# Kernel optimization log

Hardware: AMD Instinct MI355X
Metric: run time of the kernel (lower is better)

## Reference

```python
import jax, jax.numpy as jnp
import numpy as np

B, T, EMB, HEAD = 8, 2048, 1024, 1024

def setup_inputs() -> dict:
    key = jax.random.key(0)
    k1, k2, k3, k4 = jax.random.split(key, 4)
    s = 1.0 / np.sqrt(EMB)
    return {
        "x": jax.random.normal(k1, (B, T, EMB), dtype=jnp.float32),
        "Wq": jax.random.normal(k2, (HEAD, EMB), dtype=jnp.float32) * s,
        "Wk": jax.random.normal(k3, (HEAD, EMB), dtype=jnp.float32) * s,
        "Wv": jax.random.normal(k4, (HEAD, EMB), dtype=jnp.float32) * s,
    }

def reference(x, Wq, Wk, Wv):
    # Bias-free projections; torch Linear weight is [out, in] -> contract on last dim.
    q = jnp.einsum('btc,hc->bth', x, Wq)  # [B,T,HEAD]
    k = jnp.einsum('btc,hc->bth', x, Wk)
    v = jnp.einsum('btc,hc->bth', x, Wv)
    C = x.shape[-1]
    scale = jnp.asarray(C, x.dtype) ** -0.5  # NOTE: scales by emb dim C, as in source
    wei = jnp.einsum('bth,bsh->bts', q, k) * scale  # [B,T,T]
    Tn = x.shape[1]
    causal = jnp.tril(jnp.ones((Tn, Tn), dtype=bool))
    wei = jnp.where(causal, wei, -jnp.inf)
    wei = jax.nn.softmax(wei, axis=-1)
    # dropout omitted (eval mode / deterministic reference)
    out = jnp.einsum('bts,bsh->bth', wei, v)  # [B,T,HEAD]
    return out
```

## Files before the change

kernel.cpp:

```cpp
#include <hip/hip_runtime.h>

typedef unsigned short u16;
typedef short short8 __attribute__((ext_vector_type(8)));
typedef float f32x4 __attribute__((ext_vector_type(4)));

__device__ __forceinline__ u16 f2bf(float f) {
    union { float f; unsigned u; } c; c.f = f;
    unsigned r = c.u + 0x7fffu + ((c.u >> 16) & 1u);
    return (u16)(r >> 16);
}
__device__ __forceinline__ float bf2f(u16 h) {
    union { unsigned u; float f; } c; c.u = ((unsigned)h) << 16; return c.f;
}

__device__ __forceinline__ void gll16(const u16* g, u16* l) {
    __builtin_amdgcn_global_load_lds(
        (const __attribute__((address_space(1))) void*)g,
        (__attribute__((address_space(3))) void*)l, 16, 0, 0);
}

__device__ __forceinline__ void stage_half(const u16* __restrict__ g, int ld,
                                           u16* lds, int w, int lane) {
    int rowl = w * 16 + (lane >> 3);
    int s = lane & 7;
    gll16(g + (size_t)rowl * ld + ((s ^ (rowl & 7)) << 3), lds + (w * 2) * 512);
    rowl += 8;
    gll16(g + (size_t)rowl * ld + ((s ^ (rowl & 7)) << 3), lds + (w * 2 + 1) * 512);
}

__device__ __forceinline__ short8 ldsfrag(const u16* h, int row, int slot) {
    return *reinterpret_cast<const short8*>(h + row * 64 + ((slot ^ (row & 7)) << 3));
}

__device__ __forceinline__ void gemm256(
    const u16* __restrict__ A, int lda,
    const u16* __restrict__ B, int ldb,
    int m0, int n0, int nk,
    u16* Ab, u16* Bb, f32x4 acc[8][4])
{
    const int tid  = threadIdx.x;
    const int lane = tid & 63;
    const int w    = tid >> 6;
    const int wm   = w >> 2;
    const int wn   = w & 3;
    const int kg   = lane >> 4, l15 = lane & 15;

    const u16* Am = A + (size_t)m0 * lda;
    const u16* Bn = B + (size_t)n0 * ldb;

    stage_half(Am,                       lda, Ab + 0 * 8192, w, lane);
    stage_half(Am + (size_t)128 * lda,   lda, Ab + 1 * 8192, w, lane);
    stage_half(Bn,                       ldb, Bb + 0 * 8192, w, lane);
    stage_half(Bn + (size_t)128 * ldb,   ldb, Bb + 1 * 8192, w, lane);
    if (nk > 1) {
        stage_half(Bn + 64,                     ldb, Bb + 2 * 8192, w, lane);
        stage_half(Bn + (size_t)128 * ldb + 64, ldb, Bb + 3 * 8192, w, lane);
        asm volatile("s_waitcnt vmcnt(4)" ::: "memory");
    } else {
        asm volatile("s_waitcnt vmcnt(0)" ::: "memory");
    }
    __builtin_amdgcn_s_barrier();

    for (int t = 0; t < nk; ++t) {
        const int p = t & 1;
        const u16* Ahalf = Ab + (p * 2 + wm) * 8192;
        const u16* Bhalf = Bb + (p * 2 + (wn >> 1)) * 8192;
        const int brow0 = (wn & 1) * 64;
        short8 bfr[4][2];

        #pragma unroll
        for (int mp = 0; mp < 4; ++mp) {
            short8 a[2][2];
            #pragma unroll
            for (int mi = 0; mi < 2; ++mi)
                #pragma unroll
                for (int ks = 0; ks < 2; ++ks)
                    a[mi][ks] = ldsfrag(Ahalf, (mp * 2 + mi) * 16 + l15, ks * 4 + kg);
            if (mp == 0) {
                #pragma unroll
                for (int nt = 0; nt < 4; ++nt)
                    #pragma unroll
                    for (int ks = 0; ks < 2; ++ks)
                        bfr[nt][ks] = ldsfrag(Bhalf, brow0 + nt * 16 + l15, ks * 4 + kg);
            }
            if (mp == 0 && t + 1 < nk)
                stage_half(Am + (t + 1) * 64, lda, Ab + ((p ^ 1) * 2 + 0) * 8192, w, lane);
            if (mp == 1 && t + 1 < nk)
                stage_half(Am + (size_t)128 * lda + (t + 1) * 64, lda, Ab + ((p ^ 1) * 2 + 1) * 8192, w, lane);
            if (mp == 2 && t + 2 < nk)
                stage_half(Bn + (t + 2) * 64, ldb, Bb + (p * 2 + 0) * 8192, w, lane);
            if (mp == 3 && t + 2 < nk)
                stage_half(Bn + (size_t)128 * ldb + (t + 2) * 64, ldb, Bb + (p * 2 + 1) * 8192, w, lane);

            __builtin_amdgcn_s_barrier();
            __builtin_amdgcn_s_setprio(1);
            #pragma unroll
            for (int ks = 0; ks < 2; ++ks)
                #pragma unroll
                for (int mi = 0; mi < 2; ++mi)
                    #pragma unroll
                    for (int nt = 0; nt < 4; ++nt)
                        acc[mp * 2 + mi][nt] = __builtin_amdgcn_mfma_f32_16x16x32_bf16(
                            a[mi][ks], bfr[nt][ks], acc[mp * 2 + mi][nt], 0, 0, 0);
            __builtin_amdgcn_s_setprio(0);
            if (mp == 3) {
                if (t + 2 < nk) asm volatile("s_waitcnt vmcnt(4)" ::: "memory");
                else            asm volatile("s_waitcnt vmcnt(0)" ::: "memory");
            }
            __builtin_amdgcn_s_barrier();
        }
    }
}

__global__ __launch_bounds__(256) void cvt_bf16(
    const float* __restrict__ x,
    const float* __restrict__ Wq,
    const float* __restrict__ Wk,
    const float* __restrict__ Wv,
    u16* __restrict__ dst)
{
    const size_t e = ((size_t)blockIdx.x * 256 + threadIdx.x) * 8;
    const float* src;
    if (e < (size_t)16777216) {
        src = x + e;
    } else {
        size_t j = e - 16777216;
        int z = (int)(j >> 20);
        const float* Wz = (z == 0) ? Wq : (z == 1) ? Wk : Wv;
        src = Wz + (j & 1048575);
    }
    float4 a = *reinterpret_cast<const float4*>(src);
    float4 b = *reinterpret_cast<const float4*>(src + 4);
    short8 v;
    v[0] = (short)f2bf(a.x); v[1] = (short)f2bf(a.y);
    v[2] = (short)f2bf(a.z); v[3] = (short)f2bf(a.w);
    v[4] = (short)f2bf(b.x); v[5] = (short)f2bf(b.y);
    v[6] = (short)f2bf(b.z); v[7] = (short)f2bf(b.w);
    *reinterpret_cast<short8*>(dst + e) = v;
}

__global__ __launch_bounds__(512, 2) void qkv256(
    const u16* __restrict__ xb,
    const u16* __restrict__ Wb,
    u16* __restrict__ Qo, u16* __restrict__ Ko, u16* __restrict__ VTo)
{
    __shared__ u16 Ab[4][8192];
    __shared__ u16 Bb[4][8192];
    const int tid = threadIdx.x;
    const int lane = tid & 63, w = tid >> 6;
    const int wm = w >> 2, wn = w & 3, kg = lane >> 4, l15 = lane & 15;
    const int m0 = blockIdx.x * 256, n0 = blockIdx.y * 256, z = blockIdx.z;

    const f32x4 z4 = {0.f, 0.f, 0.f, 0.f};
    f32x4 acc[8][4];
    #pragma unroll
    for (int i = 0; i < 8; ++i)
        #pragma unroll
        for (int j = 0; j < 4; ++j) acc[i][j] = z4;

    gemm256(xb, 1024, Wb + (size_t)z * 1048576, 1024, m0, n0, 16, &Ab[0][0], &Bb[0][0], acc);

    if (z < 2) {
        u16* O = (z == 0) ? Qo : Ko;
        #pragma unroll
        for (int mt = 0; mt < 8; ++mt) {
            const int row0 = m0 + wm * 128 + mt * 16 + kg * 4;
            #pragma unroll
            for (int nt = 0; nt < 4; ++nt) {
                const int col = n0 + wn * 64 + nt * 16 + l15;
                #pragma unroll
                for (int r = 0; r < 4; ++r)
                    O[(size_t)(row0 + r) * 1024 + col] = f2bf(acc[mt][nt][r]);
            }
        }
    } else {
        #pragma unroll
        for (int mt = 0; mt < 8; ++mt) {
            const int row0 = m0 + wm * 128 + mt * 16 + kg * 4;
            #pragma unroll
            for (int nt = 0; nt < 4; ++nt) {
                const int col = n0 + wn * 64 + nt * 16 + l15;
                #pragma unroll
                for (int r = 0; r < 4; ++r) {
                    const int rr = row0 + r;
                    VTo[((size_t)(rr >> 11) * 1024 + col) * 2048 + (rr & 2047)] = f2bf(acc[mt][nt][r]);
                }
            }
        }
    }
}

__global__ __launch_bounds__(512, 2) void sp256(
    const u16* __restrict__ Q, const u16* __restrict__ K, u16* __restrict__ P)
{
    const int qb = blockIdx.x, kb = blockIdx.y, b = blockIdx.z;
    if (kb > qb) return;
    __shared__ u16 Ab[4][8192];
    __shared__ u16 Bb[4][8192];
    const int tid = threadIdx.x;
    const int lane = tid & 63, w = tid >> 6;
    const int wm = w >> 2, wn = w & 3, kg = lane >> 4, l15 = lane & 15;

    const f32x4 z4 = {0.f, 0.f, 0.f, 0.f};
    f32x4 acc[8][4];
    #pragma unroll
    for (int i = 0; i < 8; ++i)
        #pragma unroll
        for (int j = 0; j < 4; ++j) acc[i][j] = z4;

    gemm256(Q, 1024, K, 1024, b * 2048 + qb * 256, b * 2048 + kb * 256, 16,
            &Ab[0][0], &Bb[0][0], acc);

    u16* Pb = P + (size_t)b * 2048 * 2048;
    #pragma unroll
    for (int mt = 0; mt < 8; ++mt) {
        const int trow0 = qb * 256 + wm * 128 + mt * 16 + kg * 4;
        #pragma unroll
        for (int nt = 0; nt < 4; ++nt) {
            const int scol = kb * 256 + wn * 64 + nt * 16 + l15;
            #pragma unroll
            for (int r = 0; r < 4; ++r) {
                const int trow = trow0 + r;
                const float p = (scol <= trow) ? __expf(acc[mt][nt][r] * 0.03125f) : 0.f;
                Pb[(size_t)trow * 2048 + scol] = f2bf(p);
            }
        }
    }
}

__global__ __launch_bounds__(512, 2) void pv256(
    const u16* __restrict__ P, const u16* __restrict__ VT, float* __restrict__ Of)
{
    const int b = blockIdx.x >> 3, qblk = blockIdx.x & 7;
    const int nb = blockIdx.y;
    const int nk = (qblk + 1) * 4;
    __shared__ u16 Ab[4][8192];
    __shared__ u16 Bb[4][8192];
    const int tid = threadIdx.x;
    const int lane = tid & 63, w = tid >> 6;
    const int wm = w >> 2, wn = w & 3, kg = lane >> 4, l15 = lane & 15;

    const f32x4 z4 = {0.f, 0.f, 0.f, 0.f};
    f32x4 acc[8][4];
    #pragma unroll
    for (int i = 0; i < 8; ++i)
        #pragma unroll
        for (int j = 0; j < 4; ++j) acc[i][j] = z4;

    gemm256(P + (size_t)b * 2048 * 2048, 2048,
            VT + (size_t)b * 1024 * 2048, 2048,
            qblk * 256, nb * 256, nk, &Ab[0][0], &Bb[0][0], acc);

    #pragma unroll
    for (int mt = 0; mt < 8; ++mt) {
        const int trow0 = qblk * 256 + wm * 128 + mt * 16 + kg * 4;
        #pragma unroll
        for (int nt = 0; nt < 4; ++nt) {
            const int col = nb * 256 + wn * 64 + nt * 16 + l15;
            #pragma unroll
            for (int r = 0; r < 4; ++r)
                Of[((size_t)b * 2048 + trow0 + r) * 1024 + col] = acc[mt][nt][r];
        }
    }
}

__global__ __launch_bounds__(256) void finalize(
    const u16* __restrict__ P, const float* __restrict__ Of, float* __restrict__ out)
{
    const int row = blockIdx.x;
    const int tid = threadIdx.x;
    const int b = row >> 11, t = row & 2047;
    const int len = ((t >> 8) + 1) * 256;
    const u16* prow = P + ((size_t)b * 2048 + t) * 2048;

    float s = 0.f;
    const int i = tid * 8;
    if (i < len) {
        short8 v = *reinterpret_cast<const short8*>(prow + i);
        #pragma unroll
        for (int j = 0; j < 8; ++j) s += bf2f((u16)v[j]);
    }
    #pragma unroll
    for (int d = 1; d < 64; d <<= 1) s += __shfl_xor(s, d, 64);

    __shared__ float red[4];
    if ((tid & 63) == 0) red[tid >> 6] = s;
    __syncthreads();
    const float rinv = 1.f / (red[0] + red[1] + red[2] + red[3]);

    const size_t o = (size_t)row * 1024 + tid * 4;
    f32x4 v = *reinterpret_cast<const f32x4*>(Of + o);
    v[0] *= rinv; v[1] *= rinv; v[2] *= rinv; v[3] *= rinv;
    *reinterpret_cast<f32x4*>(out + o) = v;
}

extern "C" void kernel_launch(void* const* d_in, const int* in_sizes, int n_in,
                              void* d_out, int out_size, void* d_ws, size_t ws_size,
                              hipStream_t stream) {
    const float* x  = (const float*)d_in[0];
    const float* Wq = (const float*)d_in[1];
    const float* Wk = (const float*)d_in[2];
    const float* Wv = (const float*)d_in[3];
    float* out = (float*)d_out;

    u16* Qb  = (u16*)d_ws;
    u16* Kb  = Qb + (size_t)16384 * 1024;
    u16* VTb = Kb + (size_t)16384 * 1024;
    float* Of = (float*)d_ws;

    u16* xb = (u16*)d_out;
    u16* Wb = xb + (size_t)16777216;
    u16* Pb = (u16*)d_out;

    cvt_bf16<<<dim3(9728), 256, 0, stream>>>(x, Wq, Wk, Wv, xb);
    qkv256<<<dim3(64, 4, 3), 512, 0, stream>>>(xb, Wb, Qb, Kb, VTb);
    sp256<<<dim3(8, 8, 8), 512, 0, stream>>>(Qb, Kb, Pb);
    pv256<<<dim3(64, 4), 512, 0, stream>>>(Pb, VTb, Of);
    finalize<<<dim3(16384), 256, 0, stream>>>(Pb, Of, out);
}
```

Measured before the change: 299.8 us.

## Rework GEMM pipeline to 4-stage BK=32 and store only causal P tiles

Replaces the double-buffered BK=64 GEMM core with a 4-buffer BK=32 pipeline that keeps two register fragment sets and prefetches three stages ahead. The score kernel now writes only the lower-triangular 256x256 P tiles into a packed workspace and emits per-tile row sums. A small rowsum kernel turns those into reciprocals, and the PV kernel applies them in its epilogue, which removes the separate finalize pass and the fp32 intermediate buffer. When the workspace is large enough, V is projected after the score stage so its buffer can reuse Q's space. This adds extra kernel launches and a workspace-size-dependent code path.

```diff
diff --git a/kernel.cpp b/kernel.cpp
--- a/kernel.cpp
+++ b/kernel.cpp
@@ -3,6 +3,12 @@
 typedef unsigned short u16;
 typedef short short8 __attribute__((ext_vector_type(8)));
 typedef float f32x4 __attribute__((ext_vector_type(4)));
+
+#define WS_K_OFF    33554432ULL
+#define WS_PTRI     67108864ULL
+#define WS_PART     104857600ULL
+#define WS_RINV     105381888ULL
+#define WS_NEED     105447424ULL
 
 __device__ __forceinline__ u16 f2bf(float f) {
     union { float f; unsigned u; } c; c.f = f;
@@ -12,103 +18,96 @@
 __device__ __forceinline__ float bf2f(u16 h) {
     union { unsigned u; float f; } c; c.u = ((unsigned)h) << 16; return c.f;
 }
-
 __device__ __forceinline__ void gll16(const u16* g, u16* l) {
     __builtin_amdgcn_global_load_lds(
         (const __attribute__((address_space(1))) void*)g,
         (__attribute__((address_space(3))) void*)l, 16, 0, 0);
 }
 
-__device__ __forceinline__ void stage_half(const u16* __restrict__ g, int ld,
-                                           u16* lds, int w, int lane) {
-    int rowl = w * 16 + (lane >> 3);
-    int s = lane & 7;
-    gll16(g + (size_t)rowl * ld + ((s ^ (rowl & 7)) << 3), lds + (w * 2) * 512);
-    rowl += 8;
-    gll16(g + (size_t)rowl * ld + ((s ^ (rowl & 7)) << 3), lds + (w * 2 + 1) * 512);
-}
-
-__device__ __forceinline__ short8 ldsfrag(const u16* h, int row, int slot) {
-    return *reinterpret_cast<const short8*>(h + row * 64 + ((slot ^ (row & 7)) << 3));
-}
-
-__device__ __forceinline__ void gemm256(
+template<int AMODE>
+__device__ __forceinline__ void gemm_pipe(
     const u16* __restrict__ A, int lda,
     const u16* __restrict__ B, int ldb,
-    int m0, int n0, int nk,
-    u16* Ab, u16* Bb, f32x4 acc[8][4])
+    int m0, int n0, int nk, u16* lds, f32x4 acc[8][4])
 {
     const int tid  = threadIdx.x;
     const int lane = tid & 63;
     const int w    = tid >> 6;
-    const int wm   = w >> 2;
-    const int wn   = w & 3;
+    const int wm   = w >> 2, wn = w & 3;
     const int kg   = lane >> 4, l15 = lane & 15;
-
-    const u16* Am = A + (size_t)m0 * lda;
-    const u16* Bn = B + (size_t)n0 * ldb;
-
-    stage_half(Am,                       lda, Ab + 0 * 8192, w, lane);
-    stage_half(Am + (size_t)128 * lda,   lda, Ab + 1 * 8192, w, lane);
-    stage_half(Bn,                       ldb, Bb + 0 * 8192, w, lane);
-    stage_half(Bn + (size_t)128 * ldb,   ldb, Bb + 1 * 8192, w, lane);
-    if (nk > 1) {
-        stage_half(Bn + 64,                     ldb, Bb + 2 * 8192, w, lane);
-        stage_half(Bn + (size_t)128 * ldb + 64, ldb, Bb + 3 * 8192, w, lane);
-        asm volatile("s_waitcnt vmcnt(4)" ::: "memory");
-    } else {
-        asm volatile("s_waitcnt vmcnt(0)" ::: "memory");
-    }
+    const int r0   = w * 32 + (lane >> 2);
+    const int s0   = (lane & 3) ^ ((r0 >> 1) & 3);
+
+    const int ldA = AMODE ? 256 : lda;
+    const u16* Ar0 = A + (size_t)(m0 + r0) * ldA + s0 * 8;
+    const u16* Ar1 = Ar0 + 16 * ldA;
+    const u16* Br0 = B + (size_t)(n0 + r0) * ldb + s0 * 8;
+    const u16* Br1 = Br0 + 16 * ldb;
+
+    auto aoff = [&](int t) -> int {
+        return AMODE ? ((t >> 3) * 65536 + (t & 7) * 32) : t * 32;
+    };
+    auto STAGE = [&](int t) {
+        const int ao = aoff(t), bo = t * 32, buf = (t & 3) * 16384;
+        u16* dA = lds + buf + w * 1024;
+        u16* dB = lds + buf + 8192 + w * 1024;
+        gll16(Ar0 + ao, dA);
+        gll16(Ar1 + ao, dA + 512);
+        gll16(Br0 + bo, dB);
+        gll16(Br1 + bo, dB + 512);
+    };
+    auto LDA8 = [&](short8* fa, int t) {
+        const u16* h = lds + (t & 3) * 16384 + wm * 128 * 32;
+        #pragma unroll
+        for (int mt = 0; mt < 8; ++mt) {
+            const int row = mt * 16 + l15;
+            fa[mt] = *reinterpret_cast<const short8*>(
+                h + row * 32 + ((kg ^ ((row >> 1) & 3)) << 3));
+        }
+    };
+    auto LDB4 = [&](short8* fb, int t) {
+        const u16* h = lds + (t & 3) * 16384 + 8192 + wn * 64 * 32;
+        #pragma unroll
+        for (int nt = 0; nt < 4; ++nt) {
+            const int row = nt * 16 + l15;
+            fb[nt] = *reinterpret_cast<const short8*>(
+                h + row * 32 + ((kg ^ ((row >> 1) & 3)) << 3));
+        }
+    };
+    auto MFMA32 = [&](short8* fa, short8* fb) {
+        __builtin_amdgcn_s_setprio(1);
+        #pragma unroll
+        for (int mt = 0; mt < 8; ++mt)
+            #pragma unroll
+            for (int nt = 0; nt < 4; ++nt)
+                acc[mt][nt] = __builtin_amdgcn_mfma_f32_16x16x32_bf16(
+                    fa[mt], fb[nt], acc[mt][nt], 0, 0, 0);
+        __builtin_amdgcn_s_setprio(0);
+    };
+
+    STAGE(0); STAGE(1); STAGE(2);
+    asm volatile("s_waitcnt vmcnt(4)" ::: "memory");
     __builtin_amdgcn_s_barrier();
 
-    for (int t = 0; t < nk; ++t) {
-        const int p = t & 1;
-        const u16* Ahalf = Ab + (p * 2 + wm) * 8192;
-        const u16* Bhalf = Bb + (p * 2 + (wn >> 1)) * 8192;
-        const int brow0 = (wn & 1) * 64;
-        short8 bfr[4][2];
-
-        #pragma unroll
-        for (int mp = 0; mp < 4; ++mp) {
-            short8 a[2][2];
-            #pragma unroll
-            for (int mi = 0; mi < 2; ++mi)
-                #pragma unroll
-                for (int ks = 0; ks < 2; ++ks)
-                    a[mi][ks] = ldsfrag(Ahalf, (mp * 2 + mi) * 16 + l15, ks * 4 + kg);
-            if (mp == 0) {
-                #pragma unroll
-                for (int nt = 0; nt < 4; ++nt)
-                    #pragma unroll
-                    for (int ks = 0; ks < 2; ++ks)
-                        bfr[nt][ks] = ldsfrag(Bhalf, brow0 + nt * 16 + l15, ks * 4 + kg);
-            }
-            if (mp == 0 && t + 1 < nk)
-                stage_half(Am + (t + 1) * 64, lda, Ab + ((p ^ 1) * 2 + 0) * 8192, w, lane);
-            if (mp == 1 && t + 1 < nk)
-                stage_half(Am + (size_t)128 * lda + (t + 1) * 64, lda, Ab + ((p ^ 1) * 2 + 1) * 8192, w, lane);
-            if (mp == 2 && t + 2 < nk)
-                stage_half(Bn + (t + 2) * 64, ldb, Bb + (p * 2 + 0) * 8192, w, lane);
-            if (mp == 3 && t + 2 < nk)
-                stage_half(Bn + (size_t)128 * ldb + (t + 2) * 64, ldb, Bb + (p * 2 + 1) * 8192, w, lane);
-
-            __builtin_amdgcn_s_barrier();
-            __builtin_amdgcn_s_setprio(1);
-            #pragma unroll
-            for (int ks = 0; ks < 2; ++ks)
-                #pragma unroll
-                for (int mi = 0; mi < 2; ++mi)
-                    #pragma unroll
-                    for (int nt = 0; nt < 4; ++nt)
-                        acc[mp * 2 + mi][nt] = __builtin_amdgcn_mfma_f32_16x16x32_bf16(
-                            a[mi][ks], bfr[nt][ks], acc[mp * 2 + mi][nt], 0, 0, 0);
-            __builtin_amdgcn_s_setprio(0);
-            if (mp == 3) {
-                if (t + 2 < nk) asm volatile("s_waitcnt vmcnt(4)" ::: "memory");
-                else            asm volatile("s_waitcnt vmcnt(0)" ::: "memory");
-            }
-            __builtin_amdgcn_s_barrier();
-        }
+    short8 faA[8], faB[8], fb[4];
+    LDA8(faA, 0);
+
+    for (int t = 0; t < nk; t += 2) {
+        LDB4(fb, t);
+        LDA8(faB, t + 1);
+        if (t + 3 < nk) STAGE(t + 3);
+        MFMA32(faA, fb);
+        if (t + 3 < nk) asm volatile("s_waitcnt vmcnt(4)" ::: "memory");
+        else            asm volatile("s_waitcnt vmcnt(0)" ::: "memory");
+        __builtin_amdgcn_s_barrier();
+
+        LDB4(fb, t + 1);
+        if (t + 2 < nk) LDA8(faA, t + 2);
+        if (t + 4 < nk) STAGE(t + 4);
+        MFMA32(faB, fb);
+        if (t + 4 < nk) asm volatile("s_waitcnt vmcnt(4)" ::: "memory");
+        else            asm volatile("s_waitcnt vmcnt(0)" ::: "memory");
+        __builtin_amdgcn_s_barrier();
     }
 }
 
@@ -139,17 +138,15 @@
     *reinterpret_cast<short8*>(dst + e) = v;
 }
 
-__global__ __launch_bounds__(512, 2) void qkv256(
-    const u16* __restrict__ xb,
-    const u16* __restrict__ Wb,
-    u16* __restrict__ Qo, u16* __restrict__ Ko, u16* __restrict__ VTo)
-{
-    __shared__ u16 Ab[4][8192];
-    __shared__ u16 Bb[4][8192];
-    const int tid = threadIdx.x;
-    const int lane = tid & 63, w = tid >> 6;
+__global__ __launch_bounds__(512, 2) void qkv_pipe(
+    const u16* __restrict__ xb, const u16* __restrict__ Wb,
+    u16* __restrict__ Qo, u16* __restrict__ Ko, u16* __restrict__ VTo, int zbase)
+{
+    __shared__ u16 L[65536];
+    const int tid = threadIdx.x, lane = tid & 63, w = tid >> 6;
     const int wm = w >> 2, wn = w & 3, kg = lane >> 4, l15 = lane & 15;
-    const int m0 = blockIdx.x * 256, n0 = blockIdx.y * 256, z = blockIdx.z;
+    const int m0 = blockIdx.x * 256, n0 = blockIdx.y * 256;
+    const int z = blockIdx.z + zbase;
 
     const f32x4 z4 = {0.f, 0.f, 0.f, 0.f};
     f32x4 acc[8][4];
@@ -158,7 +155,7 @@
         #pragma unroll
         for (int j = 0; j < 4; ++j) acc[i][j] = z4;
 
-    gemm256(xb, 1024, Wb + (size_t)z * 1048576, 1024, m0, n0, 16, &Ab[0][0], &Bb[0][0], acc);
+    gemm_pipe<0>(xb, 1024, Wb + (size_t)z * 1048576, 1024, m0, n0, 32, L, acc);
 
     if (z < 2) {
         u16* O = (z == 0) ? Qo : Ko;
@@ -190,15 +187,14 @@
     }
 }
 
-__global__ __launch_bounds__(512, 2) void sp256(
-    const u16* __restrict__ Q, const u16* __restrict__ K, u16* __restrict__ P)
+__global__ __launch_bounds__(512, 2) void sp_new(
+    const u16* __restrict__ Q, const u16* __restrict__ K,
+    u16* __restrict__ Ptri, float* __restrict__ partials)
 {
     const int qb = blockIdx.x, kb = blockIdx.y, b = blockIdx.z;
     if (kb > qb) return;
-    __shared__ u16 Ab[4][8192];
-    __shared__ u16 Bb[4][8192];
-    const int tid = threadIdx.x;
-    const int lane = tid & 63, w = tid >> 6;
+    __shared__ u16 L[65536];
+    const int tid = threadIdx.x, lane = tid & 63, w = tid >> 6;
     const int wm = w >> 2, wn = w & 3, kg = lane >> 4, l15 = lane & 15;
 
     const f32x4 z4 = {0.f, 0.f, 0.f, 0.f};
@@ -208,8 +204,55 @@
         #pragma unroll
         for (int j = 0; j < 4; ++j) acc[i][j] = z4;
 
-    gemm256(Q, 1024, K, 1024, b * 2048 + qb * 256, b * 2048 + kb * 256, 16,
-            &Ab[0][0], &Bb[0][0], acc);
+    gemm_pipe<0>(Q, 1024, K, 1024, b * 2048 + qb * 256, b * 2048 + kb * 256, 32, L, acc);
+
+    u16* Pt = Ptri + ((size_t)b * 36 + (qb * (qb + 1)) / 2 + kb) * 65536;
+    float* psum = (float*)L;
+    #pragma unroll
+    for (int mt = 0; mt < 8; ++mt) {
+        const int lt0 = wm * 128 + mt * 16 + kg * 4;
+        #pragma unroll
+        for (int r = 0; r < 4; ++r) {
+            const int lt = lt0 + r;
+            const int gt = qb * 256 + lt;
+            float ps = 0.f;
+            #pragma unroll
+            for (int nt = 0; nt < 4; ++nt) {
+                const int lcol = wn * 64 + nt * 16 + l15;
+                const int gs = kb * 256 + lcol;
+                const float p = (gs <= gt) ? __expf(acc[mt][nt][r] * 0.03125f) : 0.f;
+                ps += p;
+                Pt[(size_t)lt * 256 + lcol] = f2bf(p);
+            }
+            #pragma unroll
+            for (int d = 1; d < 16; d <<= 1) ps += __shfl_xor(ps, d, 64);
+            if (l15 == 0) psum[lt * 4 + wn] = ps;
+        }
+    }
+    __syncthreads();
+    if (tid < 256) {
+        const float s = psum[tid * 4] + psum[tid * 4 + 1] + psum[tid * 4 + 2] + psum[tid * 4 + 3];
+        partials[((size_t)b * 2048 + qb * 256 + tid) * 8 + kb] = s;
+    }
+}
+
+__global__ __launch_bounds__(512, 2) void sp_old(
+    const u16* __restrict__ Q, const u16* __restrict__ K, u16* __restrict__ P)
+{
+    const int qb = blockIdx.x, kb = blockIdx.y, b = blockIdx.z;
+    if (kb > qb) return;
+    __shared__ u16 L[65536];
+    const int tid = threadIdx.x, lane = tid & 63, w = tid >> 6;
+    const int wm = w >> 2, wn = w & 3, kg = lane >> 4, l15 = lane & 15;
+
+    const f32x4 z4 = {0.f, 0.f, 0.f, 0.f};
+    f32x4 acc[8][4];
+    #pragma unroll
+    for (int i = 0; i < 8; ++i)
+        #pragma unroll
+        for (int j = 0; j < 4; ++j) acc[i][j] = z4;
+
+    gemm_pipe<0>(Q, 1024, K, 1024, b * 2048 + qb * 256, b * 2048 + kb * 256, 32, L, acc);
 
     u16* Pb = P + (size_t)b * 2048 * 2048;
     #pragma unroll
@@ -228,16 +271,25 @@
     }
 }
 
-__global__ __launch_bounds__(512, 2) void pv256(
-    const u16* __restrict__ P, const u16* __restrict__ VT, float* __restrict__ Of)
+__global__ __launch_bounds__(256) void rowsum_k(
+    const float* __restrict__ partials, float* __restrict__ rinv)
+{
+    const int row = blockIdx.x * 256 + threadIdx.x;
+    const int qb = (row & 2047) >> 8;
+    float s = 0.f;
+    for (int kb = 0; kb <= qb; ++kb) s += partials[(size_t)row * 8 + kb];
+    rinv[row] = 1.f / s;
+}
+
+__global__ __launch_bounds__(512, 2) void pv_new(
+    const u16* __restrict__ Ptri, const u16* __restrict__ VT,
+    const float* __restrict__ rinv, float* __restrict__ out)
 {
     const int b = blockIdx.x >> 3, qblk = blockIdx.x & 7;
     const int nb = blockIdx.y;
-    const int nk = (qblk + 1) * 4;
-    __shared__ u16 Ab[4][8192];
-    __shared__ u16 Bb[4][8192];
-    const int tid = threadIdx.x;
-    const int lane = tid & 63, w = tid >> 6;
+    const int nk = (qblk + 1) * 8;
+    __shared__ u16 L[65536];
+    const int tid = threadIdx.x, lane = tid & 63, w = tid >> 6;
     const int wm = w >> 2, wn = w & 3, kg = lane >> 4, l15 = lane & 15;
 
     const f32x4 z4 = {0.f, 0.f, 0.f, 0.f};
@@ -247,9 +299,46 @@
         #pragma unroll
         for (int j = 0; j < 4; ++j) acc[i][j] = z4;
 
-    gemm256(P + (size_t)b * 2048 * 2048, 2048,
-            VT + (size_t)b * 1024 * 2048, 2048,
-            qblk * 256, nb * 256, nk, &Ab[0][0], &Bb[0][0], acc);
+    const u16* Aq = Ptri + ((size_t)b * 36 + (qblk * (qblk + 1)) / 2) * 65536;
+    gemm_pipe<1>(Aq, 256, VT + (size_t)b * 1024 * 2048, 2048, 0, nb * 256, nk, L, acc);
+
+    #pragma unroll
+    for (int mt = 0; mt < 8; ++mt) {
+        const int lt0 = wm * 128 + mt * 16 + kg * 4;
+        const int grow0 = b * 2048 + qblk * 256 + lt0;
+        float rs[4];
+        #pragma unroll
+        for (int r = 0; r < 4; ++r) rs[r] = rinv[grow0 + r];
+        #pragma unroll
+        for (int nt = 0; nt < 4; ++nt) {
+            const int col = nb * 256 + wn * 64 + nt * 16 + l15;
+            #pragma unroll
+            for (int r = 0; r < 4; ++r)
+                out[(size_t)(grow0 + r) * 1024 + col] = acc[mt][nt][r] * rs[r];
+        }
+    }
+}
+
+__global__ __launch_bounds__(512, 2) void pv_old(
+    const u16* __restrict__ P, const u16* __restrict__ VT, float* __restrict__ Of)
+{
+    const int b = blockIdx.x >> 3, qblk = blockIdx.x & 7;
+    const int nb = blockIdx.y;
+    const int nk = (qblk + 1) * 8;
+    __shared__ u16 L[65536];
+    const int tid = threadIdx.x, lane = tid & 63, w = tid >> 6;
+    const int wm = w >> 2, wn = w & 3, kg = lane >> 4, l15 = lane & 15;
+
+    const f32x4 z4 = {0.f, 0.f, 0.f, 0.f};
+    f32x4 acc[8][4];
+    #pragma unroll
+    for (int i = 0; i < 8; ++i)
+        #pragma unroll
+        for (int j = 0; j < 4; ++j) acc[i][j] = z4;
+
+    gemm_pipe<0>(P + (size_t)b * 2048 * 2048, 2048,
+                 VT + (size_t)b * 1024 * 2048, 2048,
+                 qblk * 256, nb * 256, nk, L, acc);
 
     #pragma unroll
     for (int mt = 0; mt < 8; ++mt) {
@@ -301,20 +390,35 @@
     const float* Wq = (const float*)d_in[1];
     const float* Wk = (const float*)d_in[2];
     const float* Wv = (const float*)d_in[3];
-    float* out = (float*)d_out;
-
-    u16* Qb  = (u16*)d_ws;
-    u16* Kb  = Qb + (size_t)16384 * 1024;
-    u16* VTb = Kb + (size_t)16384 * 1024;
-    float* Of = (float*)d_ws;
 
     u16* xb = (u16*)d_out;
     u16* Wb = xb + (size_t)16777216;
-    u16* Pb = (u16*)d_out;
 
     cvt_bf16<<<dim3(9728), 256, 0, stream>>>(x, Wq, Wk, Wv, xb);
-    qkv256<<<dim3(64, 4, 3), 512, 0, stream>>>(xb, Wb, Qb, Kb, VTb);
-    sp256<<<dim3(8, 8, 8), 512, 0, stream>>>(Qb, Kb, Pb);
-    pv256<<<dim3(64, 4), 512, 0, stream>>>(Pb, VTb, Of);
-    finalize<<<dim3(16384), 256, 0, stream>>>(Pb, Of, out);
-}
+
+    if (ws_size >= WS_NEED) {
+        u16*   Qb   = (u16*)d_ws;
+        u16*   Kb   = (u16*)((char*)d_ws + WS_K_OFF);
+        u16*   Pt   = (u16*)((char*)d_ws + WS_PTRI);
+        float* part = (float*)((char*)d_ws + WS_PART);
+        float* rinv = (float*)((char*)d_ws + WS_RINV);
+        u16*   VTb  = Qb;
+
+        qkv_pipe<<<dim3(64, 4, 2), 512, 0, stream>>>(xb, Wb, Qb, Kb, Qb, 0);
+        sp_new<<<dim3(8, 8, 8), 512, 0, stream>>>(Qb, Kb, Pt, part);
+        rowsum_k<<<dim3(64), 256, 0, stream>>>(part, rinv);
+        qkv_pipe<<<dim3(64, 4, 1), 512, 0, stream>>>(xb, Wb, Qb, Kb, VTb, 2);
+        pv_new<<<dim3(64, 4), 512, 0, stream>>>(Pt, VTb, rinv, (float*)d_out);
+    } else {
+        u16* Qb  = (u16*)d_ws;
+        u16* Kb  = Qb + (size_t)16384 * 1024;
+        u16* VTb = Kb + (size_t)16384 * 1024;
+        float* Of = (float*)d_ws;
+        u16* Pb = (u16*)d_out;
+
+        qkv_pipe<<<dim3(64, 4, 3), 512, 0, stream>>>(xb, Wb, Qb, Kb, VTb, 0);
+        sp_old<<<dim3(8, 8, 8), 512, 0, stream>>>(Qb, Kb, Pb);
+        pv_old<<<dim3(64, 4), 512, 0, stream>>>(Pb, VTb, Of);
+        finalize<<<dim3(16384), 256, 0, stream>>>(Pb, Of, (float*)d_out);
+    }
+}
```

Result: faster. 267.2 us (-10.9%).
